# Kernel tuning notes

Measured on AMD Instinct MI355X. Metric: run time of the kernel, lower is better.

Reference implementation:

```python
import jax, jax.numpy as jnp
import numpy as np

D_MODEL, N_HEADS, D_FF = 512, 8, 2048
D_K = D_MODEL // N_HEADS
EPS = 1e-5


def layer_norm(x, g, b):
    mu = jnp.mean(x, axis=-1, keepdims=True)
    var = jnp.mean(jnp.square(x - mu), axis=-1, keepdims=True)
    return (x - mu) * jax.lax.rsqrt(var + EPS) * g + b


def setup_inputs() -> dict:
    key = jax.random.key(0)
    ks = jax.random.split(key, 12)
    B, S = 2, 2048
    s_attn = 1.0 / np.sqrt(D_MODEL)
    s_ff1 = 1.0 / np.sqrt(D_MODEL)
    s_ff2 = 1.0 / np.sqrt(D_FF)
    inp = {
        "x": jax.random.normal(ks[0], (B, S, D_MODEL), dtype=jnp.float32),
        "mask": jnp.ones((B, 1, 1, S), dtype=jnp.int32),
        "Wq": jax.random.normal(ks[1], (D_MODEL, D_MODEL), jnp.float32) * s_attn,
        "bq": jnp.zeros((D_MODEL,), jnp.float32),
        "Wk": jax.random.normal(ks[2], (D_MODEL, D_MODEL), jnp.float32) * s_attn,
        "bk": jnp.zeros((D_MODEL,), jnp.float32),
        "Wv": jax.random.normal(ks[3], (D_MODEL, D_MODEL), jnp.float32) * s_attn,
        "bv": jnp.zeros((D_MODEL,), jnp.float32),
        "Wo": jax.random.normal(ks[4], (D_MODEL, D_MODEL), jnp.float32) * s_attn,
        "bo": jnp.zeros((D_MODEL,), jnp.float32),
        "W1": jax.random.normal(ks[5], (D_MODEL, D_FF), jnp.float32) * s_ff1,
        "b1": jnp.zeros((D_FF,), jnp.float32),
        "W2": jax.random.normal(ks[6], (D_FF, D_MODEL), jnp.float32) * s_ff2,
        "b2": jnpp.zeros((D_MODEL,), jnp.float32) if False else jnp.zeros((D_MODEL,), jnp.float32),
        "g1": jnp.ones((D_MODEL,), jnp.float32),
        "beta1": jnp.zeros((D_MODEL,), jnp.float32),
        "g2": jnp.ones((D_MODEL,), jnp.float32),
        "beta2": jnp.zeros((D_MODEL,), jnp.float32),
    }
    return inp


def reference(x, mask, Wq, bq, Wk, bk, Wv, bv, Wo, bo, W1, b1, W2, b2, g1, beta1, g2, beta2):
    B, S, _ = x.shape
    # projections -> [B, H, S, Dk]
    def split_heads(t):
        return t.reshape(B, S, N_HEADS, D_K).transpose(0, 2, 1, 3)
    q = split_heads(x @ Wq + bq)
    k = split_heads(x @ Wk + bk)
    v = split_heads(x @ Wv + bv)
    scores = jnp.einsum("bhqd,bhkd->bhqk", q, k) / np.sqrt(D_K)
    scores = jnp.where(mask == 0, jnp.float32(-1e9), scores)
    attn = jax.nn.softmax(scores, axis=-1)
    ctx = jnp.einsum("bhqk,bhkd->bhqd", attn, v)
    ctx = ctx.transpose(0, 2, 1, 3).reshape(B, S, D_MODEL)
    attn_out = ctx @ Wo + bo
    x1 = layer_norm(x + attn_out, g1, beta1)
    ff = jax.nn.relu(x1 @ W1 + b1) @ W2 + b2
    return layer_norm(x1 + ff, g2, beta2)
```

## Files before the change

kernel.cpp:

```cpp
#include <hip/hip_runtime.h>
#include <hip/hip_bf16.h>


#define D_MODEL 512
#define N_HEADS 8
#define D_K 64
#define D_FF 2048
#define BATCH 2
#define SEQ 2048
#define NROWS (BATCH * SEQ)

typedef __hip_bfloat16 bf16;
typedef __attribute__((ext_vector_type(8))) short bf16x8;
typedef __attribute__((ext_vector_type(4))) float f32x4;

__device__ __forceinline__ unsigned short f2b(float f) {
  union { bf16 b; unsigned short u; } cv;
  cv.b = __float2bfloat16(f);
  return cv.u;
}
__device__ __forceinline__ float b2f(unsigned short u) {
  return __uint_as_float(((unsigned int)u) << 16);
}
__device__ __forceinline__ float toF(const bf16 x) { return __bfloat162float(x); }
__device__ __forceinline__ float toF(const float x) { return x; }
__device__ __forceinline__ void storeC(float* p, float v) { *p = v; }
__device__ __forceinline__ void storeC(bf16* p, float v) {
  *p = __float2bfloat16(v);
}

__device__ __forceinline__ void ld8f(const float* p, float* v) {
  const float4 a = *(const float4*)p;
  const float4 b = *(const float4*)(p + 4);
  v[0] = a.x; v[1] = a.y; v[2] = a.z; v[3] = a.w;
  v[4] = b.x; v[5] = b.y; v[6] = b.z; v[7] = b.w;
}
__device__ __forceinline__ void ld8f(const bf16* p, float* v) {
  const bf16x8 u = *(const bf16x8*)p;
#pragma unroll
  for (int i = 0; i < 8; ++i) v[i] = b2f((unsigned short)u[i]);
}
__device__ __forceinline__ void st8f(float* p, const float* v) {
  *(float4*)p = make_float4(v[0], v[1], v[2], v[3]);
  *(float4*)(p + 4) = make_float4(v[4], v[5], v[6], v[7]);
}
__device__ __forceinline__ void st8f(bf16* p, const float* v) {
  bf16x8 u;
#pragma unroll
  for (int i = 0; i < 8; ++i) u[i] = (short)f2b(v[i]);
  *(bf16x8*)p = u;
}

#define WT_Q 0
#define WT_K 262144
#define WT_V 524288
#define WT_O 786432
#define WT_1 1048576
#define WT_2 2097152

__global__ __launch_bounds__(256) void prep_kernel(
    const float* __restrict__ Wq, const float* __restrict__ Wk,
    const float* __restrict__ Wv, const float* __restrict__ Wo,
    const float* __restrict__ W1, const float* __restrict__ W2,
    bf16* __restrict__ outw, const float* __restrict__ x,
    bf16* __restrict__ xb) {
  const int z = blockIdx.z;
  const int t = threadIdx.x;

  if (z == 6) {
    const size_t base =
        ((size_t)(blockIdx.y * 32 + blockIdx.x) * 2048) + (size_t)t * 8;
    float v[8];
    ld8f(x + base, v);
    st8f(xb + base, v);
    return;
  }

  const float* W;
  int R, Cn;
  size_t off;
  if (z == 0)      { W = Wq; R = 512;  Cn = 512;  off = WT_Q; }
  else if (z == 1) { W = Wk; R = 512;  Cn = 512;  off = WT_K; }
  else if (z == 2) { W = Wv; R = 512;  Cn = 512;  off = WT_V; }
  else if (z == 3) { W = Wo; R = 512;  Cn = 512;  off = WT_O; }
  else if (z == 4) { W = W1; R = 512;  Cn = 2048; off = WT_1; }
  else             { W = W2; R = 2048; Cn = 512;  off = WT_2; }
  const int c0 = blockIdx.x * 64;
  const int r0 = blockIdx.y * 64;
  if (c0 >= Cn || r0 >= R) return;

  __shared__ short tile[64][72];
  {
    const int r = t >> 2, cg = (t & 3) * 16;
    const float* src = &W[(size_t)(r0 + r) * Cn + c0 + cg];
#pragma unroll
    for (int i = 0; i < 4; ++i) {
      const float4 v = *(const float4*)(src + 4 * i);
      tile[cg + 4 * i + 0][r] = (short)f2b(v.x);
      tile[cg + 4 * i + 1][r] = (short)f2b(v.y);
      tile[cg + 4 * i + 2][r] = (short)f2b(v.z);
      tile[cg + 4 * i + 3][r] = (short)f2b(v.w);
    }
  }
  __syncthreads();
  {
    const int c = t >> 2, rg = (t & 3) * 16;
    short* dst = (short*)outw + off + (size_t)(c0 + c) * R + r0 + rg;
    *(bf16x8*)dst = *(const bf16x8*)&tile[c][rg];
    *(bf16x8*)(dst + 8) = *(const bf16x8*)&tile[c][rg + 8];
  }
}

template <int BM, int BN, bool RELU, bool RESID>
__global__ __launch_bounds__(256) void gemm_bf16_kernel(
    const bf16* __restrict__ A, int lda,
    const bf16* __restrict__ Wt0, const bf16* __restrict__ Wt1,
    const bf16* __restrict__ Wt2, int ldk,
    const float* __restrict__ b0, const float* __restrict__ b1,
    const float* __restrict__ b2,
    bf16* __restrict__ C0, bf16* __restrict__ C1, bf16* __restrict__ C2,
    int ldc, int K, const bf16* __restrict__ R) {
  const bf16* Wt = (blockIdx.z == 0) ? Wt0 : (blockIdx.z == 1 ? Wt1 : Wt2);
  const float* bias = (blockIdx.z == 0) ? b0 : (blockIdx.z == 1 ? b1 : b2);
  bf16* C = (blockIdx.z == 0) ? C0 : (blockIdx.z == 1 ? C1 : C2);

  constexpr int WX = BN / 64;
  constexpr int WY = 4 / WX;
  constexpr int RG = BM / (16 * WY);
  constexpr int NA = BM / 32;
  constexpr int NW = BN / 32;

  __shared__ short as_[BM][72];
  __shared__ short bs[BN][72];

  const int rowBase = blockIdx.y * BM;
  const int colBase = blockIdx.x * BN;
  const int t = threadIdx.x;
  const int wave = t >> 6;
  const int lane = t & 63;
  const int quad = lane >> 4;
  const int l15 = lane & 15;
  const int wy = wave / WX;
  const int wx = wave % WX;

  const int arow = (NA == 2) ? (t >> 2) : (t >> 1);
  const int akc = (NA == 2) ? ((t & 3) * 16) : ((t & 1) * 32);
  const int wrow = (NW == 2) ? (t >> 2) : (t >> 1);
  const int wkc = (NW == 2) ? ((t & 3) * 16) : ((t & 1) * 32);

  const short* Abase = (const short*)A + (size_t)(rowBase + arow) * lda + akc;
  const short* Wbase = (const short*)Wt + (size_t)(colBase + wrow) * ldk + wkc;

  bf16x8 areg[NA], wreg[NW];
#pragma unroll
  for (int i = 0; i < NA; ++i) areg[i] = *(const bf16x8*)(Abase + 8 * i);
#pragma unroll
  for (int i = 0; i < NW; ++i) wreg[i] = *(const bf16x8*)(Wbase + 8 * i);

  f32x4 acc[RG][4];
#pragma unroll
  for (int i = 0; i < RG; ++i)
#pragma unroll
    for (int nt = 0; nt < 4; ++nt) acc[i][nt] = (f32x4){0.f, 0.f, 0.f, 0.f};

  for (int k0 = 0; k0 < K; k0 += 64) {
#pragma unroll
    for (int i = 0; i < NA; ++i) *(bf16x8*)&as_[arow][akc + 8 * i] = areg[i];
#pragma unroll
    for (int i = 0; i < NW; ++i) *(bf16x8*)&bs[wrow][wkc + 8 * i] = wreg[i];

    if (k0 + 64 < K) {
#pragma unroll
      for (int i = 0; i < NA; ++i)
        areg[i] = *(const bf16x8*)(Abase + k0 + 64 + 8 * i);
#pragma unroll
      for (int i = 0; i < NW; ++i)
        wreg[i] = *(const bf16x8*)(Wbase + k0 + 64 + 8 * i);
    }
    __syncthreads();

#pragma unroll
    for (int kc = 0; kc < 2; ++kc) {
      bf16x8 af[RG];
#pragma unroll
      for (int i = 0; i < RG; ++i)
        af[i] = *(const bf16x8*)
            &as_[wy * (16 * RG) + i * 16 + l15][quad * 8 + kc * 32];
#pragma unroll
      for (int nt = 0; nt < 4; ++nt) {
        const bf16x8 bfr = *(const bf16x8*)
            &bs[wx * 64 + nt * 16 + l15][quad * 8 + kc * 32];
#pragma unroll
        for (int i = 0; i < RG; ++i)
          acc[i][nt] = __builtin_amdgcn_mfma_f32_16x16x32_bf16(
              af[i], bfr, acc[i][nt], 0, 0, 0);
      }
    }
    __syncthreads();
  }

#pragma unroll
  for (int i = 0; i < RG; ++i)
#pragma unroll
    for (int nt = 0; nt < 4; ++nt) {
      const int col = colBase + wx * 64 + nt * 16 + l15;
#pragma unroll
      for (int r = 0; r < 4; ++r) {
        const int row = rowBase + wy * (16 * RG) + i * 16 + quad * 4 + r;
        float v = acc[i][nt][r] + bias[col];
        if (RESID) v += toF(R[(size_t)row * ldc + col]);
        if (RELU) v = fmaxf(v, 0.f);
        storeC(&C[(size_t)row * ldc + col], v);
      }
    }
}

__global__ __launch_bounds__(512) void attn_mfma_kernel(
    const bf16* __restrict__ Q, const bf16* __restrict__ Km,
    const bf16* __restrict__ V, const int* __restrict__ mask,
    bf16* __restrict__ ctx) {
  const int qt = blockIdx.x;
  const int bh = blockIdx.y;
  const int b = bh >> 3;
  const int h = bh & 7;
  const int t = threadIdx.x;
  const int wave = t >> 6;
  const int half = wave >> 2;
  const int wq = wave & 3;
  const int lane = t & 63;
  const int quad = lane >> 4;
  const int l15 = lane & 15;

  __shared__ __align__(16) char smem[74240];
  auto ks = (short(*)[64][72])(smem);
  auto vt = (short(*)[64][72])(smem + 18432);
  auto pb = (short(*)[32][72])(smem + 36864);
  auto mk = (int(*)[64])(smem + 73728);
  auto mg = (float(*)[32][68])(smem);

  bf16x8 qf[2][2];
#pragma unroll
  for (int rg = 0; rg < 2; ++rg) {
    const short* qg = (const short*)Q +
        (size_t)(b * SEQ + qt * 128 + wq * 32 + rg * 16 + l15) * D_MODEL +
        h * D_K + quad * 8;
    qf[rg][0] = *(const bf16x8*)qg;
    qf[rg][1] = *(const bf16x8*)(qg + 32);
  }

  f32x4 of[2][4];
#pragma unroll
  for (int rg = 0; rg < 2; ++rg)
#pragma unroll
    for (int nt = 0; nt < 4; ++nt) of[rg][nt] = (f32x4){0.f, 0.f, 0.f, 0.f};
  float l_acc[2][4] = {{0.f, 0.f, 0.f, 0.f}, {0.f, 0.f, 0.f, 0.f}};

  const int hs = t >> 8;
  const int tt = t & 255;
  const int kr = tt >> 2, kc0 = (tt & 3) * 16;
  const int vk = tt & 63, vc0 = ((tt >> 6) & 3) * 16;

  bf16x8 kv0, kv1, vv0, vv1;
  int mv = 1;
  {
    const int keyRow = (hs * 16 + 0) * 64;
    const short* kg = (const short*)Km +
        (size_t)(b * SEQ + keyRow + kr) * D_MODEL + h * D_K + kc0;
    kv0 = *(const bf16x8*)kg;
    kv1 = *(const bf16x8*)(kg + 8);
    const short* vg = (const short*)V +
        (size_t)(b * SEQ + keyRow + vk) * D_MODEL + h * D_K + vc0;
    vv0 = *(const bf16x8*)vg;
    vv1 = *(const bf16x8*)(vg + 8);
    if (tt < 64) mv = mask[b * SEQ + keyRow + tt];
  }

  for (int kt = 0; kt < 16; ++kt) {
    *(bf16x8*)&ks[hs][kr][kc0] = kv0;
    *(bf16x8*)&ks[hs][kr][kc0 + 8] = kv1;
#pragma unroll
    for (int i = 0; i < 8; ++i) vt[hs][vc0 + i][vk] = vv0[i];
#pragma unroll
    for (int i = 0; i < 8; ++i) vt[hs][vc0 + 8 + i][vk] = vv1[i];
    if (tt < 64) mk[hs][tt] = mv;

    if (kt + 1 < 16) {
      const int keyRow = (hs * 16 + kt + 1) * 64;
      const short* kg = (const short*)Km +
          (size_t)(b * SEQ + keyRow + kr) * D_MODEL + h * D_K + kc0;
      kv0 = *(const bf16x8*)kg;
      kv1 = *(const bf16x8*)(kg + 8);
      const short* vg = (const short*)V +
          (size_t)(b * SEQ + keyRow + vk) * D_MODEL + h * D_K + vc0;
      vv0 = *(const bf16x8*)vg;
      vv1 = *(const bf16x8*)(vg + 8);
      if (tt < 64) mv = mask[b * SEQ + keyRow + tt];
    }
    __syncthreads();

    f32x4 sf[2][4];
#pragma unroll
    for (int nt = 0; nt < 4; ++nt) {
      const bf16x8 kf0 = *(const bf16x8*)&ks[half][l15 + 16 * nt][quad * 8];
      const bf16x8 kf1 =
          *(const bf16x8*)&ks[half][l15 + 16 * nt][quad * 8 + 32];
#pragma unroll
      for (int rg = 0; rg < 2; ++rg) {
        f32x4 acc = (f32x4){0.f, 0.f, 0.f, 0.f};
        acc = __builtin_amdgcn_mfma_f32_16x16x32_bf16(qf[rg][0], kf0, acc, 0, 0, 0);
        acc = __builtin_amdgcn_mfma_f32_16x16x32_bf16(qf[rg][1], kf1, acc, 0, 0, 0);
        sf[rg][nt] = acc;
      }
    }

#pragma unroll
    for (int nt = 0; nt < 4; ++nt) {
      const bool dead = (mk[half][l15 + 16 * nt] == 0);
#pragma unroll
      for (int rg = 0; rg < 2; ++rg)
#pragma unroll
        for (int r = 0; r < 4; ++r) {
          float p = __expf(fmaf(sf[rg][nt][r], 0.125f, -8.f));
          if (dead) p = 0.f;
          l_acc[rg][r] += p;
          pb[wave][rg * 16 + quad * 4 + r][l15 + 16 * nt] = (short)f2b(p);
        }
    }

#pragma unroll
    for (int kc = 0; kc < 2; ++kc) {
      bf16x8 pf[2];
#pragma unroll
      for (int rg = 0; rg < 2; ++rg)
        pf[rg] = *(const bf16x8*)&pb[wave][rg * 16 + l15][kc * 32 + quad * 8];
#pragma unroll
      for (int nt = 0; nt < 4; ++nt) {
        const bf16x8 vf =
            *(const bf16x8*)&vt[half][l15 + 16 * nt][kc * 32 + quad * 8];
#pragma unroll
        for (int rg = 0; rg < 2; ++rg)
          of[rg][nt] = __builtin_amdgcn_mfma_f32_16x16x32_bf16(
              pf[rg], vf, of[rg][nt], 0, 0, 0);
      }
    }
    __syncthreads();
  }

#pragma unroll
  for (int xm = 1; xm < 16; xm <<= 1)
#pragma unroll
    for (int rg = 0; rg < 2; ++rg)
#pragma unroll
      for (int r = 0; r < 4; ++r)
        l_acc[rg][r] += __shfl_xor(l_acc[rg][r], xm, 64);

#pragma unroll
  for (int rg = 0; rg < 2; ++rg)
#pragma unroll
    for (int nt = 0; nt < 4; ++nt)
#pragma unroll
      for (int r = 0; r < 4; ++r)
        mg[wave][rg * 16 + quad * 4 + r][l15 + 16 * nt] = of[rg][nt][r];
  if (l15 == 0) {
#pragma unroll
    for (int rg = 0; rg < 2; ++rg)
#pragma unroll
      for (int r = 0; r < 4; ++r)
        mg[wave][rg * 16 + quad * 4 + r][64] = l_acc[rg][r];
  }
  __syncthreads();

  if (wave < 4) {
    const int pw = wave + 4;
#pragma unroll
    for (int rg = 0; rg < 2; ++rg)
#pragma unroll
      for (int r = 0; r < 4; ++r) {
        const int qrow = rg * 16 + quad * 4 + r;
        const float inv = 1.f / (l_acc[rg][r] + mg[pw][qrow][64]);
        const int row = qt * 128 + wave * 32 + qrow;
        bf16* cp = ctx + (size_t)(b * SEQ + row) * D_MODEL + h * D_K;
#pragma unroll
        for (int nt = 0; nt < 4; ++nt)
          cp[l15 + 16 * nt] = __float2bfloat16(
              (of[rg][nt][r] + mg[pw][qrow][l15 + 16 * nt]) * inv);
      }
  }
}

template <typename BT, typename OT>
__global__ __launch_bounds__(256) void ln_kernel(
    const BT* __restrict__ base, const float* __restrict__ g,
    const float* __restrict__ beta, OT* __restrict__ out) {
  const int wave = threadIdx.x >> 6;
  const int lane = threadIdx.x & 63;
  const int row = blockIdx.x * 4 + wave;
  const size_t rb = (size_t)row * D_MODEL + lane * 8;

  float v[8];
  ld8f(base + rb, v);

  float s = 0.f;
#pragma unroll
  for (int i = 0; i < 8; ++i) s += v[i];
#pragma unroll
  for (int xm = 1; xm < 64; xm <<= 1) s += __shfl_xor(s, xm, 64);
  const float mu = s * (1.f / (float)D_MODEL);

  float q = 0.f;
#pragma unroll
  for (int i = 0; i < 8; ++i) {
    v[i] -= mu;
    q += v[i] * v[i];
  }
#pragma unroll
  for (int xm = 1; xm < 64; xm <<= 1) q += __shfl_xor(q, xm, 64);
  const float rs = rsqrtf(q * (1.f / (float)D_MODEL) + 1e-5f);

  float gv[8], bv[8];
  ld8f(g + lane * 8, gv);
  ld8f(beta + lane * 8, bv);
#pragma unroll
  for (int i = 0; i < 8; ++i) v[i] = v[i] * rs * gv[i] + bv[i];
  st8f(out + rb, v);
}

extern "C" void kernel_launch(void* const* d_in, const int* in_sizes, int n_in,
                              void* d_out, int out_size, void* d_ws, size_t ws_size,
                              hipStream_t stream) {
  const float* x     = (const float*)d_in[0];
  const int*   mask  = (const int*)d_in[1];
  const float* Wq    = (const float*)d_in[2];
  const float* bq    = (const float*)d_in[3];
  const float* Wk    = (const float*)d_in[4];
  const float* bk    = (const float*)d_in[5];
  const float* Wv    = (const float*)d_in[6];
  const float* bv    = (const float*)d_in[7];
  const float* Wo    = (const float*)d_in[8];
  const float* bo    = (const float*)d_in[9];
  const float* W1    = (const float*)d_in[10];
  const float* b1    = (const float*)d_in[11];
  const float* W2    = (const float*)d_in[12];
  const float* b2    = (const float*)d_in[13];
  const float* g1    = (const float*)d_in[14];
  const float* beta1 = (const float*)d_in[15];
  const float* g2    = (const float*)d_in[16];
  const float* beta2 = (const float*)d_in[17];
  float* out = (float*)d_out;

  char* ws = (char*)d_ws;
  const size_t MB4 = (size_t)NROWS * D_MODEL * sizeof(bf16);
  bf16* q        = (bf16*)(ws + 0 * MB4);
  bf16* kbuf     = (bf16*)(ws + 1 * MB4);
  bf16* vbuf     = (bf16*)(ws + 2 * MB4);
  bf16* ctx      = (bf16*)(ws + 3 * MB4);
  bf16* xb       = (bf16*)(ws + 4 * MB4);
  bf16* attn_out = q;
  bf16* x1       = kbuf;
  bf16* ffacc    = vbuf;
  bf16* ffmid    = (bf16*)(ws + 4 * MB4);

  bf16* wt = (bf16*)d_out;

  const dim3 blk(256);

  prep_kernel<<<dim3(32, 32, 7), blk, 0, stream>>>(Wq, Wk, Wv, Wo, W1, W2, wt,
                                                   x, xb);

  gemm_bf16_kernel<64, 128, false, false>
      <<<dim3(D_MODEL / 128, NROWS / 64, 3), blk, 0, stream>>>(
          xb, D_MODEL, wt + WT_Q, wt + WT_K, wt + WT_V, D_MODEL,
          bq, bk, bv, q, kbuf, vbuf, D_MODEL, D_MODEL, nullptr);

  attn_mfma_kernel<<<dim3(SEQ / 128, BATCH * N_HEADS), dim3(512), 0, stream>>>(
      q, kbuf, vbuf, mask, ctx);

  gemm_bf16_kernel<64, 64, false, true>
      <<<dim3(D_MODEL / 64, NROWS / 64, 1), blk, 0, stream>>>(
          ctx, D_MODEL, wt + WT_O, wt + WT_O, wt + WT_O, D_MODEL,
          bo, bo, bo, attn_out, attn_out, attn_out, D_MODEL, D_MODEL, xb);

  ln_kernel<bf16, bf16><<<NROWS / 4, blk, 0, stream>>>(attn_out, g1, beta1, x1);

  gemm_bf16_kernel<64, 128, true, false>
      <<<dim3(D_FF / 128, NROWS / 64, 1), blk, 0, stream>>>(
          x1, D_MODEL, wt + WT_1, wt + WT_1, wt + WT_1, D_MODEL,
          b1, b1, b1, ffmid, ffmid, ffmid, D_FF, D_MODEL, nullptr);

  gemm_bf16_kernel<64, 64, false, true>
      <<<dim3(D_MODEL / 64, NROWS / 64, 1), blk, 0, stream>>>(
          ffmid, D_FF, wt + WT_2, wt + WT_2, wt + WT_2, D_FF,
          b2, b2, b2, ffacc, ffacc, ffacc, D_MODEL, D_FF, x1);

  ln_kernel<bf16, float><<<NROWS / 4, blk, 0, stream>>>(ffacc, g2, beta2, out);
}
```

Before: 205.2 us.

## Load GEMM MFMA fragments directly from global into registers, skipping LDS

Rewrites the bf16 GEMM so each wave loads its A and W MFMA fragments directly from global memory into a two-stage register double buffer, removing the shared-memory tiles and block barriers. The K loop becomes a compile-time trip count (NS) and is fully unrolled. This removes LDS writes/reads and synchronisation but loses cross-wave data reuse, so the same tiles are fetched multiple times from cache, and it raises register usage.

```diff
diff --git a/kernel.cpp b/kernel.cpp
--- a/kernel.cpp
+++ b/kernel.cpp
@@ -111,7 +111,7 @@
   }
 }
 
-template <int BM, int BN, bool RELU, bool RESID>
+template <int BM, int BN, int NS, bool RELU, bool RESID>
 __global__ __launch_bounds__(256) void gemm_bf16_kernel(
     const bf16* __restrict__ A, int lda,
     const bf16* __restrict__ Wt0, const bf16* __restrict__ Wt1,
@@ -119,7 +119,7 @@
     const float* __restrict__ b0, const float* __restrict__ b1,
     const float* __restrict__ b2,
     bf16* __restrict__ C0, bf16* __restrict__ C1, bf16* __restrict__ C2,
-    int ldc, int K, const bf16* __restrict__ R) {
+    int ldc, const bf16* __restrict__ R) {
   const bf16* Wt = (blockIdx.z == 0) ? Wt0 : (blockIdx.z == 1 ? Wt1 : Wt2);
   const float* bias = (blockIdx.z == 0) ? b0 : (blockIdx.z == 1 ? b1 : b2);
   bf16* C = (blockIdx.z == 0) ? C0 : (blockIdx.z == 1 ? C1 : C2);
@@ -127,11 +127,6 @@
   constexpr int WX = BN / 64;
   constexpr int WY = 4 / WX;
   constexpr int RG = BM / (16 * WY);
-  constexpr int NA = BM / 32;
-  constexpr int NW = BN / 32;
-
-  __shared__ short as_[BM][72];
-  __shared__ short bs[BN][72];
 
   const int rowBase = blockIdx.y * BM;
   const int colBase = blockIdx.x * BN;
@@ -143,19 +138,33 @@
   const int wy = wave / WX;
   const int wx = wave % WX;
 
-  const int arow = (NA == 2) ? (t >> 2) : (t >> 1);
-  const int akc = (NA == 2) ? ((t & 3) * 16) : ((t & 1) * 32);
-  const int wrow = (NW == 2) ? (t >> 2) : (t >> 1);
-  const int wkc = (NW == 2) ? ((t & 3) * 16) : ((t & 1) * 32);
-
-  const short* Abase = (const short*)A + (size_t)(rowBase + arow) * lda + akc;
-  const short* Wbase = (const short*)Wt + (size_t)(colBase + wrow) * ldk + wkc;
-
-  bf16x8 areg[NA], wreg[NW];
-#pragma unroll
-  for (int i = 0; i < NA; ++i) areg[i] = *(const bf16x8*)(Abase + 8 * i);
-#pragma unroll
-  for (int i = 0; i < NW; ++i) wreg[i] = *(const bf16x8*)(Wbase + 8 * i);
+  const short* aP[RG];
+#pragma unroll
+  for (int i = 0; i < RG; ++i)
+    aP[i] = (const short*)A +
+            (size_t)(rowBase + wy * (16 * RG) + i * 16 + l15) * lda + quad * 8;
+  const short* bP[4];
+#pragma unroll
+  for (int nt = 0; nt < 4; ++nt)
+    bP[nt] = (const short*)Wt +
+             (size_t)(colBase + wx * 64 + nt * 16 + l15) * ldk + quad * 8;
+
+  bf16x8 af[2][RG][2];
+  bf16x8 bfr[2][4][2];
+
+#pragma unroll
+  for (int s = 0; s < 2; ++s) {
+#pragma unroll
+    for (int i = 0; i < RG; ++i)
+#pragma unroll
+      for (int kc = 0; kc < 2; ++kc)
+        af[s][i][kc] = *(const bf16x8*)(aP[i] + s * 64 + kc * 32);
+#pragma unroll
+    for (int nt = 0; nt < 4; ++nt)
+#pragma unroll
+      for (int kc = 0; kc < 2; ++kc)
+        bfr[s][nt][kc] = *(const bf16x8*)(bP[nt] + s * 64 + kc * 32);
+  }
 
   f32x4 acc[RG][4];
 #pragma unroll
@@ -163,40 +172,29 @@
 #pragma unroll
     for (int nt = 0; nt < 4; ++nt) acc[i][nt] = (f32x4){0.f, 0.f, 0.f, 0.f};
 
-  for (int k0 = 0; k0 < K; k0 += 64) {
-#pragma unroll
-    for (int i = 0; i < NA; ++i) *(bf16x8*)&as_[arow][akc + 8 * i] = areg[i];
-#pragma unroll
-    for (int i = 0; i < NW; ++i) *(bf16x8*)&bs[wrow][wkc + 8 * i] = wreg[i];
-
-    if (k0 + 64 < K) {
-#pragma unroll
-      for (int i = 0; i < NA; ++i)
-        areg[i] = *(const bf16x8*)(Abase + k0 + 64 + 8 * i);
-#pragma unroll
-      for (int i = 0; i < NW; ++i)
-        wreg[i] = *(const bf16x8*)(Wbase + k0 + 64 + 8 * i);
-    }
-    __syncthreads();
-
-#pragma unroll
-    for (int kc = 0; kc < 2; ++kc) {
-      bf16x8 af[RG];
-#pragma unroll
-      for (int i = 0; i < RG; ++i)
-        af[i] = *(const bf16x8*)
-            &as_[wy * (16 * RG) + i * 16 + l15][quad * 8 + kc * 32];
-#pragma unroll
-      for (int nt = 0; nt < 4; ++nt) {
-        const bf16x8 bfr = *(const bf16x8*)
-            &bs[wx * 64 + nt * 16 + l15][quad * 8 + kc * 32];
+#pragma unroll
+  for (int s = 0; s < NS; ++s) {
+    const int cur = s & 1;
+#pragma unroll
+    for (int kc = 0; kc < 2; ++kc)
+#pragma unroll
+      for (int nt = 0; nt < 4; ++nt)
 #pragma unroll
         for (int i = 0; i < RG; ++i)
           acc[i][nt] = __builtin_amdgcn_mfma_f32_16x16x32_bf16(
-              af[i], bfr, acc[i][nt], 0, 0, 0);
-      }
-    }
-    __syncthreads();
+              af[cur][i][kc], bfr[cur][nt][kc], acc[i][nt], 0, 0, 0);
+    if (s + 2 < NS) {
+#pragma unroll
+      for (int i = 0; i < RG; ++i)
+#pragma unroll
+        for (int kc = 0; kc < 2; ++kc)
+          af[cur][i][kc] = *(const bf16x8*)(aP[i] + (s + 2) * 64 + kc * 32);
+#pragma unroll
+      for (int nt = 0; nt < 4; ++nt)
+#pragma unroll
+        for (int kc = 0; kc < 2; ++kc)
+          bfr[cur][nt][kc] = *(const bf16x8*)(bP[nt] + (s + 2) * 64 + kc * 32);
+    }
   }
 
 #pragma unroll
@@ -467,30 +465,30 @@
   prep_kernel<<<dim3(32, 32, 7), blk, 0, stream>>>(Wq, Wk, Wv, Wo, W1, W2, wt,
                                                    x, xb);
 
-  gemm_bf16_kernel<64, 128, false, false>
+  gemm_bf16_kernel<64, 128, 8, false, false>
       <<<dim3(D_MODEL / 128, NROWS / 64, 3), blk, 0, stream>>>(
           xb, D_MODEL, wt + WT_Q, wt + WT_K, wt + WT_V, D_MODEL,
-          bq, bk, bv, q, kbuf, vbuf, D_MODEL, D_MODEL, nullptr);
+          bq, bk, bv, q, kbuf, vbuf, D_MODEL, nullptr);
 
   attn_mfma_kernel<<<dim3(SEQ / 128, BATCH * N_HEADS), dim3(512), 0, stream>>>(
       q, kbuf, vbuf, mask, ctx);
 
-  gemm_bf16_kernel<64, 64, false, true>
+  gemm_bf16_kernel<64, 64, 8, false, true>
       <<<dim3(D_MODEL / 64, NROWS / 64, 1), blk, 0, stream>>>(
           ctx, D_MODEL, wt + WT_O, wt + WT_O, wt + WT_O, D_MODEL,
-          bo, bo, bo, attn_out, attn_out, attn_out, D_MODEL, D_MODEL, xb);
+          bo, bo, bo, attn_out, attn_out, attn_out, D_MODEL, xb);
 
   ln_kernel<bf16, bf16><<<NROWS / 4, blk, 0, stream>>>(attn_out, g1, beta1, x1);
 
-  gemm_bf16_kernel<64, 128, true, false>
+  gemm_bf16_kernel<64, 128, 8, true, false>
       <<<dim3(D_FF / 128, NROWS / 64, 1), blk, 0, stream>>>(
           x1, D_MODEL, wt + WT_1, wt + WT_1, wt + WT_1, D_MODEL,
-          b1, b1, b1, ffmid, ffmid, ffmid, D_FF, D_MODEL, nullptr);
-
-  gemm_bf16_kernel<64, 64, false, true>
+          b1, b1, b1, ffmid, ffmid, ffmid, D_FF, nullptr);
+
+  gemm_bf16_kernel<64, 64, 32, false, true>
       <<<dim3(D_MODEL / 64, NROWS / 64, 1), blk, 0, stream>>>(
           ffmid, D_FF, wt + WT_2, wt + WT_2, wt + WT_2, D_FF,
-          b2, b2, b2, ffacc, ffacc, ffacc, D_MODEL, D_FF, x1);
+          b2, b2, b2, ffacc, ffacc, ffacc, D_MODEL, x1);
 
   ln_kernel<bf16, float><<<NROWS / 4, blk, 0, stream>>>(ffacc, g2, beta2, out);
 }
```

Result: slower. 330.7 us (+61.1%).

## Write V transposed per head from QKV GEMM epilogue for attention

Applied to the files above, without the earlier changes.

The QKV projection GEMM now writes the V output in a transposed [B,H,Dk,S] layout, storing 4 consecutive keys per lane. The attention kernel then loads V tiles with vector stores into shared memory instead of scattering 16 scalar shared-memory writes per thread to transpose them. This moves the transpose cost from the attention inner loop to the GEMM epilogue, where the global writes are narrower (8-byte, strided by sequence length). It uses a new workspace region at offset 5*MB4.

```diff
diff --git a/kernel.cpp b/kernel.cpp
--- a/kernel.cpp
+++ b/kernel.cpp
@@ -12,6 +12,7 @@
 
 typedef __hip_bfloat16 bf16;
 typedef __attribute__((ext_vector_type(8))) short bf16x8;
+typedef __attribute__((ext_vector_type(4))) short bf16x4;
 typedef __attribute__((ext_vector_type(4))) float f32x4;
 
 __device__ __forceinline__ unsigned short f2b(float f) {
@@ -111,7 +112,7 @@
   }
 }
 
-template <int BM, int BN, bool RELU, bool RESID>
+template <int BM, int BN, bool RELU, bool RESID, bool TRV>
 __global__ __launch_bounds__(256) void gemm_bf16_kernel(
     const bf16* __restrict__ A, int lda,
     const bf16* __restrict__ Wt0, const bf16* __restrict__ Wt1,
@@ -199,6 +200,25 @@
     __syncthreads();
   }
 
+  if (TRV && blockIdx.z == 2) {
+#pragma unroll
+    for (int i = 0; i < RG; ++i)
+#pragma unroll
+      for (int nt = 0; nt < 4; ++nt) {
+        const int col = colBase + wx * 64 + nt * 16 + l15;
+        const int h_ = col >> 6, d_ = col & 63;
+        const int row0 = rowBase + wy * (16 * RG) + i * 16 + quad * 4;
+        const int b_ = row0 >> 11, k0_ = row0 & 2047;
+        const float bia = bias[col];
+        bf16x4 u;
+#pragma unroll
+        for (int r = 0; r < 4; ++r) u[r] = (short)f2b(acc[i][nt][r] + bia);
+        *(bf16x4*)((unsigned short*)C +
+                   ((size_t)((b_ * 8 + h_) * 64 + d_)) * 2048 + k0_) = u;
+      }
+    return;
+  }
+
 #pragma unroll
   for (int i = 0; i < RG; ++i)
 #pragma unroll
@@ -217,7 +237,7 @@
 
 __global__ __launch_bounds__(512) void attn_mfma_kernel(
     const bf16* __restrict__ Q, const bf16* __restrict__ Km,
-    const bf16* __restrict__ V, const int* __restrict__ mask,
+    const bf16* __restrict__ Vt_g, const int* __restrict__ mask,
     bf16* __restrict__ ctx) {
   const int qt = blockIdx.x;
   const int bh = blockIdx.y;
@@ -258,7 +278,8 @@
   const int hs = t >> 8;
   const int tt = t & 255;
   const int kr = tt >> 2, kc0 = (tt & 3) * 16;
-  const int vk = tt & 63, vc0 = ((tt >> 6) & 3) * 16;
+
+  const short* VtRow = (const short*)Vt_g + (size_t)(bh * 64 + kr) * 2048;
 
   bf16x8 kv0, kv1, vv0, vv1;
   int mv = 1;
@@ -268,8 +289,7 @@
         (size_t)(b * SEQ + keyRow + kr) * D_MODEL + h * D_K + kc0;
     kv0 = *(const bf16x8*)kg;
     kv1 = *(const bf16x8*)(kg + 8);
-    const short* vg = (const short*)V +
-        (size_t)(b * SEQ + keyRow + vk) * D_MODEL + h * D_K + vc0;
+    const short* vg = VtRow + keyRow + kc0;
     vv0 = *(const bf16x8*)vg;
     vv1 = *(const bf16x8*)(vg + 8);
     if (tt < 64) mv = mask[b * SEQ + keyRow + tt];
@@ -278,10 +298,8 @@
   for (int kt = 0; kt < 16; ++kt) {
     *(bf16x8*)&ks[hs][kr][kc0] = kv0;
     *(bf16x8*)&ks[hs][kr][kc0 + 8] = kv1;
-#pragma unroll
-    for (int i = 0; i < 8; ++i) vt[hs][vc0 + i][vk] = vv0[i];
-#pragma unroll
-    for (int i = 0; i < 8; ++i) vt[hs][vc0 + 8 + i][vk] = vv1[i];
+    *(bf16x8*)&vt[hs][kr][kc0] = vv0;
+    *(bf16x8*)&vt[hs][kr][kc0 + 8] = vv1;
     if (tt < 64) mk[hs][tt] = mv;
 
     if (kt + 1 < 16) {
@@ -290,8 +308,7 @@
           (size_t)(b * SEQ + keyRow + kr) * D_MODEL + h * D_K + kc0;
       kv0 = *(const bf16x8*)kg;
       kv1 = *(const bf16x8*)(kg + 8);
-      const short* vg = (const short*)V +
-          (size_t)(b * SEQ + keyRow + vk) * D_MODEL + h * D_K + vc0;
+      const short* vg = VtRow + keyRow + kc0;
       vv0 = *(const bf16x8*)vg;
       vv1 = *(const bf16x8*)(vg + 8);
       if (tt < 64) mv = mask[b * SEQ + keyRow + tt];
@@ -455,6 +472,7 @@
   bf16* vbuf     = (bf16*)(ws + 2 * MB4);
   bf16* ctx      = (bf16*)(ws + 3 * MB4);
   bf16* xb       = (bf16*)(ws + 4 * MB4);
+  bf16* vtbuf    = (bf16*)(ws + 5 * MB4);
   bf16* attn_out = q;
   bf16* x1       = kbuf;
   bf16* ffacc    = vbuf;
@@ -467,27 +485,27 @@
   prep_kernel<<<dim3(32, 32, 7), blk, 0, stream>>>(Wq, Wk, Wv, Wo, W1, W2, wt,
                                                    x, xb);
 
-  gemm_bf16_kernel<64, 128, false, false>
+  gemm_bf16_kernel<64, 128, false, false, true>
       <<<dim3(D_MODEL / 128, NROWS / 64, 3), blk, 0, stream>>>(
           xb, D_MODEL, wt + WT_Q, wt + WT_K, wt + WT_V, D_MODEL,
-          bq, bk, bv, q, kbuf, vbuf, D_MODEL, D_MODEL, nullptr);
+          bq, bk, bv, q, kbuf, vtbuf, D_MODEL, D_MODEL, nullptr);
 
   attn_mfma_kernel<<<dim3(SEQ / 128, BATCH * N_HEADS), dim3(512), 0, stream>>>(
-      q, kbuf, vbuf, mask, ctx);
-
-  gemm_bf16_kernel<64, 64, false, true>
+      q, kbuf, vtbuf, mask, ctx);
+
+  gemm_bf16_kernel<64, 64, false, true, false>
       <<<dim3(D_MODEL / 64, NROWS / 64, 1), blk, 0, stream>>>(
           ctx, D_MODEL, wt + WT_O, wt + WT_O, wt + WT_O, D_MODEL,
           bo, bo, bo, attn_out, attn_out, attn_out, D_MODEL, D_MODEL, xb);
 
   ln_kernel<bf16, bf16><<<NROWS / 4, blk, 0, stream>>>(attn_out, g1, beta1, x1);
 
-  gemm_bf16_kernel<64, 128, true, false>
+  gemm_bf16_kernel<64, 128, true, false, false>
       <<<dim3(D_FF / 128, NROWS / 64, 1), blk, 0, stream>>>(
           x1, D_MODEL, wt + WT_1, wt + WT_1, wt + WT_1, D_MODEL,
           b1, b1, b1, ffmid, ffmid, ffmid, D_FF, D_MODEL, nullptr);
 
-  gemm_bf16_kernel<64, 64, false, true>
+  gemm_bf16_kernel<64, 64, false, true, false>
       <<<dim3(D_MODEL / 64, NROWS / 64, 1), blk, 0, stream>>>(
           ffmid, D_FF, wt + WT_2, wt + WT_2, wt + WT_2, D_FF,
           b2, b2, b2, ffacc, ffacc, ffacc, D_MODEL, D_FF, x1);
```

New measurement: 202.9 us. Within noise of the previous version (-1.1%).
